# Performance work log

Hardware: AMD Instinct MI355X
Metric: run time of the kernel (lower is better)

Reference implementation:

```python
import jax, jax.numpy as jnp
import numpy as np

BETA = 0.9
THRESHOLD = 1.0
DELTA_THRESH = 0.2  # spikegen.delta threshold in encoder
NUM_STEPS = 64


def heaviside(v):
    return (v > 0).astype(v.dtype)


def lif_layer(cur):
    """snntorch Leaky (reset_mechanism='subtract') over cur: [S, B, H].
    mem_new = beta*mem + cur - (mem_old > thr)*thr ; spk = (mem_new > thr)."""
    def step(mem, c):
        reset = heaviside(mem - THRESHOLD)
        mem_new = BETA * mem + c - reset * THRESHOLD
        spk = heaviside(mem_new - THRESHOLD)
        return mem_new, spk

    mem0 = jnp.zeros(cur.shape[1:], cur.dtype)
    _, spk_rec = jax.lax.scan(step, mem0, cur)
    return spk_rec  # [S, B, H]


def setup_inputs() -> dict:
    key = jax.random.key(0)
    ks = jax.random.split(key, 7)
    F_in, H1, H2, H3 = 512, 1024, 1024, 512
    x = jax.random.normal(ks[0], (256, 128, F_in), dtype=jnp.float32)
    def lin(k, out_d, in_d):
        kw, kb = jax.random.split(k)
        s = 1.0 / np.sqrt(in_d)
        W = jax.random.uniform(kw, (out_d, in_d), jnp.float32, -s, s)
        b = jax.random.uniform(kb, (out_d,), jnp.float32, -s, s)
        return W, b
    W0, b0 = lin(ks[1], H1, F_in)
    W1, b1 = lin(ks[2], H2, H1)
    W2, b2 = lin(ks[3], H3, H2)
    return {"x": x, "W0": W0, "b0": b0, "W1": W1, "b1": b1, "W2": W2, "b2": b2}


def reference(x, W0, b0, W1, b1, W2, b2):
    B, T, F_in = x.shape
    # SpikeEncoder 'delta': spikegen.delta diffs along dim 0 (batch here, faithful to torch call)
    prev = jnp.concatenate([x[:1], x[:-1]], axis=0)
    delta_spk = ((x - prev) >= DELTA_THRESH).astype(x.dtype)  # [B, T, F]
    # repeat over S then mean over T  ==  mean over T then broadcast over S
    spikes = jnp.broadcast_to(delta_spk.mean(axis=1), (NUM_STEPS, B, F_in))  # [S, B, F]
    for W, b in ((W0, b0), (W1, b1), (W2, b2)):
        cur = jnp.einsum('sbf,hf->sbh', spikes, W) + b  # batched fc across all steps
        spikes = lif_layer(cur)
    return spikes  # [S, B, H_last]
```

## Files before the change

### kernel.cpp

```cpp
#include <hip/hip_runtime.h>
#include <hip/hip_bf16.h>

#define S_STEPS 64

typedef __bf16 bf16x8 __attribute__((ext_vector_type(8)));
typedef float  f32x4  __attribute__((ext_vector_type(4)));
typedef int    i32x4  __attribute__((ext_vector_type(4)));

__device__ __forceinline__ void async16(const void* g, void* l) {
    __builtin_amdgcn_global_load_lds((const __attribute__((address_space(1))) void*)g,
                                     (__attribute__((address_space(3))) void*)l,
                                     16, 0, 0);
}

__global__ void snn_encoder_tp(const float4* __restrict__ xv, ushort4* __restrict__ r,
                               int B, int T, int F4) {
    const int f4i = threadIdx.x & 63;
    const int tc  = threadIdx.x >> 6;
    const int b   = blockIdx.y;
    const int f4  = blockIdx.x * 64 + f4i;
    __shared__ int4 red[4][64];

    int c0 = 0, c1 = 0, c2 = 0, c3 = 0;
    if (b > 0) {
        const float4* xb = xv + ((size_t)b * T + tc * 32) * F4 + f4;
        const float4* xp = xb - (size_t)T * F4;
        for (int t = 0; t < 32; ++t) {
            float4 a = xb[(size_t)t * F4];
            float4 p = xp[(size_t)t * F4];
            c0 += (__fsub_rn(a.x, p.x) >= 0.2f) ? 1 : 0;
            c1 += (__fsub_rn(a.y, p.y) >= 0.2f) ? 1 : 0;
            c2 += (__fsub_rn(a.z, p.z) >= 0.2f) ? 1 : 0;
            c3 += (__fsub_rn(a.w, p.w) >= 0.2f) ? 1 : 0;
        }
    }
    red[tc][f4i] = int4{c0, c1, c2, c3};
    __syncthreads();
    if (tc == 0) {
        int4 a = red[0][f4i], bb = red[1][f4i], cc = red[2][f4i], dd = red[3][f4i];
        int s0 = a.x + bb.x + cc.x + dd.x;
        int s1 = a.y + bb.y + cc.y + dd.y;
        int s2 = a.z + bb.z + cc.z + dd.z;
        int s3 = a.w + bb.w + cc.w + dd.w;
        ushort4 o;
        o.x = __hip_bfloat16_raw(__float2bfloat16((float)s0 * (1.0f / 128.0f))).x;
        o.y = __hip_bfloat16_raw(__float2bfloat16((float)s1 * (1.0f / 128.0f))).x;
        o.z = __hip_bfloat16_raw(__float2bfloat16((float)s2 * (1.0f / 128.0f))).x;
        o.w = __hip_bfloat16_raw(__float2bfloat16((float)s3 * (1.0f / 128.0f))).x;
        r[(size_t)b * F4 + f4] = o;
    }
}

__global__ void split_w0_v4(const float4* __restrict__ W, int n4, ushort4* __restrict__ out) {
    int j = blockIdx.x * blockDim.x + threadIdx.x;
    if (j >= n4) return;
    float4 w = W[j];
    float wv[4] = {w.x, w.y, w.z, w.w};
    unsigned short hv[4], mv[4], lv[4];
    #pragma unroll
    for (int q = 0; q < 4; ++q) {
        __hip_bfloat16 hh = __float2bfloat16(wv[q]);
        float r1 = __fsub_rn(wv[q], __bfloat162float(hh));
        __hip_bfloat16 mm = __float2bfloat16(r1);
        float r2 = __fsub_rn(r1, __bfloat162float(mm));
        hv[q] = __hip_bfloat16_raw(hh).x;
        mv[q] = __hip_bfloat16_raw(mm).x;
        lv[q] = __hip_bfloat16_raw(__float2bfloat16(r2)).x;
    }
    out[j]          = ushort4{hv[0], hv[1], hv[2], hv[3]};
    out[j + n4]     = ushort4{mv[0], mv[1], mv[2], mv[3]};
    out[j + 2 * n4] = ushort4{lv[0], lv[1], lv[2], lv[3]};
}

__global__ void quant_w_i8(const float4* __restrict__ Wa, const float4* __restrict__ Wb,
                           int na4, int nb4,
                           char4* __restrict__ outA, char4* __restrict__ outB) {
    int i = blockIdx.x * blockDim.x + threadIdx.x;
    const float4* W; char4* out; int n4; int j = i;
    if (j < na4) { W = Wa; out = outA; n4 = na4; }
    else {
        j -= na4;
        if (j >= nb4) return;
        W = Wb; out = outB; n4 = nb4;
    }
    float4 w = W[j];
    float wv[4] = {w.x, w.y, w.z, w.w};
    signed char d2v[4], d1v[4], d0v[4];
    #pragma unroll
    for (int q = 0; q < 4; ++q) {
        int e  = __float2int_rn(wv[q] * 134217728.0f);
        int d0 = (int)(signed char)(e & 0xff);
        int e1 = (e - d0) >> 8;
        int d1 = (int)(signed char)(e1 & 0xff);
        int d2 = (e1 - d1) >> 8;
        d0v[q] = (signed char)d0;
        d1v[q] = (signed char)d1;
        d2v[q] = (signed char)d2;
    }
    out[j]          = make_char4(d2v[0], d2v[1], d2v[2], d2v[3]);
    out[j + n4]     = make_char4(d1v[0], d1v[1], d1v[2], d1v[3]);
    out[j + 2 * n4] = make_char4(d0v[0], d0v[1], d0v[2], d0v[3]);
}


__global__ __launch_bounds__(256, 2)
void snn_gemm_i8_w_lif(const signed char* __restrict__ A,
                       const signed char* __restrict__ Wq,
                       const float* __restrict__ bias,
                       signed char* __restrict__ Sout,
                       int M, int N, int K) {
    __shared__ __align__(16) char As[3 * 8192];
    __shared__ __align__(16) char Bs[3 * 16384];
    const int t    = threadIdx.x;
    const int wave = t >> 6;
    const int lane = t & 63;

    int m_idx, n_idx;
    {
        int gx = gridDim.x, gy = gridDim.y;
        int flat = blockIdx.y * gx + blockIdx.x;
        if ((gy & 7) == 0) {
            int x = flat & 7, local = flat >> 3, h = gy >> 3;
            m_idx = x * h + (local % h);
            n_idx = local / h;
        } else { m_idx = blockIdx.y; n_idx = blockIdx.x; }
    }
    const int m0 = m_idx * 128;
    const int n0 = n_idx * 256;
    const int wm = (wave >> 1) * 64;
    const int wn = (wave & 1) * 128;

    const int srow = lane >> 2;
    const int schk = ((lane & 3) + (lane >> 2) + (lane >> 4)) & 3;
    const int rho  = lane & 15;
    const int kap  = lane >> 4;
    const int foff = ((rho << 2) + ((kap - rho - (rho >> 2)) & 3)) * 16;

    const int KT = K >> 6;
    const int NT = 3 * KT;
    const size_t PK = (size_t)N * K;

    size_t aOff[2], bOff[4];
    #pragma unroll
    for (int q = 0; q < 2; ++q)
        aOff[q] = (size_t)(m0 + (wave * 2 + q) * 16 + srow) * K + schk * 16;
    #pragma unroll
    for (int q = 0; q < 4; ++q)
        bOff[q] = (size_t)(n0 + (wave * 4 + q) * 16 + srow) * K + schk * 16;

    i32x4 acc[4][8] = {};
    i32x4 afA[4], afB[4], bLo[4], bHi[4];

    auto stageT = [&](int p, int kt, int bsel) {
        const int kk = kt << 6;
        char* as = As + bsel * 8192;
        char* bs = Bs + bsel * 16384;
        #pragma unroll
        for (int q = 0; q < 2; ++q)
            async16(A + aOff[q] + kk, as + (wave * 2 + q) * 1024 + lane * 16);
        const signed char* Bw = Wq + (size_t)p * PK;
        #pragma unroll
        for (int q = 0; q < 4; ++q)
            async16(Bw + bOff[q] + kk, bs + (wave * 4 + q) * 1024 + lane * 16);
    };

    int sp = 0, skt = 2;
    int sbuf = 2, rbuf = 1;

    auto body = [&](int i, i32x4* afc, i32x4* afn) {
        if (i + 2 < NT) {
            stageT(sp, skt, sbuf);
            if (++skt == KT) { skt = 0; ++sp; }
            asm volatile("s_waitcnt vmcnt(6)" ::: "memory");
        } else {
            asm volatile("s_waitcnt vmcnt(0)" ::: "memory");
        }
        __builtin_amdgcn_s_barrier();
        const char* as = As + rbuf * 8192;
        const char* bs = Bs + rbuf * 16384;
        #pragma unroll
        for (int q = 0; q < 4; ++q)
            afn[q] = *(const i32x4*)&as[((wm >> 4) + q) * 1024 + foff];
        #pragma unroll
        for (int q = 0; q < 4; ++q)
            bLo[q] = *(const i32x4*)&bs[((wn >> 4) + q) * 1024 + foff];
        __builtin_amdgcn_sched_barrier(0);
        #pragma unroll
        for (int q = 0; q < 4; ++q)
            #pragma unroll
            for (int j = 0; j < 4; ++j)
                acc[q][4 + j] = __builtin_amdgcn_mfma_i32_16x16x64_i8(afc[q], bHi[j], acc[q][4 + j], 0, 0, 0);
        #pragma unroll
        for (int q = 0; q < 4; ++q)
            bHi[q] = *(const i32x4*)&bs[((wn >> 4) + 4 + q) * 1024 + foff];
        asm volatile("s_waitcnt lgkmcnt(0)" ::: "memory");
        __builtin_amdgcn_sched_barrier(0);
        if (((i + 1) & (KT - 1)) == 0) {
            #pragma unroll
            for (int q = 0; q < 4; ++q)
                #pragma unroll
                for (int j = 0; j < 8; ++j)
                    acc[q][j] = acc[q][j] * 256;
        }
        #pragma unroll
        for (int q = 0; q < 4; ++q)
            #pragma unroll
            for (int j = 0; j < 4; ++j)
                acc[q][j] = __builtin_amdgcn_mfma_i32_16x16x64_i8(afn[q], bLo[j], acc[q][j], 0, 0, 0);
        sbuf = (sbuf == 2) ? 0 : sbuf + 1;
        rbuf = (rbuf == 2) ? 0 : rbuf + 1;
    };

    stageT(0, 0, 0);
    stageT(0, 1, 1);
    asm volatile("s_waitcnt vmcnt(6)" ::: "memory");
    __builtin_amdgcn_s_barrier();
    {
        const char* as = As;
        const char* bs = Bs;
        #pragma unroll
        for (int q = 0; q < 4; ++q)
            afA[q] = *(const i32x4*)&as[((wm >> 4) + q) * 1024 + foff];
        #pragma unroll
        for (int q = 0; q < 4; ++q) {
            bLo[q] = *(const i32x4*)&bs[((wn >> 4) + q) * 1024 + foff];
            bHi[q] = *(const i32x4*)&bs[((wn >> 4) + 4 + q) * 1024 + foff];
        }
    }
    asm volatile("s_waitcnt lgkmcnt(0)" ::: "memory");
    __builtin_amdgcn_sched_barrier(0);
    #pragma unroll
    for (int q = 0; q < 4; ++q)
        #pragma unroll
        for (int j = 0; j < 4; ++j)
            acc[q][j] = __builtin_amdgcn_mfma_i32_16x16x64_i8(afA[q], bLo[j], acc[q][j], 0, 0, 0);

    for (int i = 0; i < NT - 2; i += 2) {
        body(i, afA, afB);
        body(i + 1, afB, afA);
    }
    body(NT - 2, afA, afB);
    #pragma unroll
    for (int q = 0; q < 4; ++q)
        #pragma unroll
        for (int j = 0; j < 4; ++j)
            acc[q][4 + j] = __builtin_amdgcn_mfma_i32_16x16x64_i8(afB[q], bHi[j], acc[q][4 + j], 0, 0, 0);

    const float SCALE = 7.450580596923828e-9f;
    float bb[8];
    #pragma unroll
    for (int j = 0; j < 8; ++j)
        bb[j] = bias[n0 + wn + j * 16 + (lane & 15)];
    #pragma unroll
    for (int i = 0; i < 4; ++i)
        #pragma unroll
        for (int j = 0; j < 8; ++j) {
            i32x4 v = acc[i][j];
            f32x4 c;
            #pragma unroll
            for (int r = 0; r < 4; ++r)
                c[r] = (float)v[r] * SCALE + bb[j];
            acc[i][j] = __builtin_bit_cast(i32x4, c);
        }
    float mj[8] = {0.f, 0.f, 0.f, 0.f, 0.f, 0.f, 0.f, 0.f};
    signed char* So = Sout + (size_t)(m0 + wm) * N;
    #pragma unroll
    for (int seg = 0; seg < 16; ++seg) {
        const int si = seg >> 2, sk = seg & 3;
        const int src = (lane & 15) | (((sk + 3) & 3) << 4);
        #pragma unroll
        for (int j = 0; j < 8; ++j) {
            float tin = __shfl(mj[j], src);
            if (seg > 0 && kap == sk) mj[j] = tin;
        }
        if (kap == sk) {
            #pragma unroll
            for (int j = 0; j < 8; ++j) {
                f32x4 c = __builtin_bit_cast(f32x4, acc[si][j]);
                const int ng = n0 + wn + j * 16 + (lane & 15);
                #pragma unroll
                for (int r = 0; r < 4; ++r) {
                    float rst = (mj[j] > 1.0f) ? 1.0f : 0.0f;
                    mj[j] = __fsub_rn(__fadd_rn(__fmul_rn(0.9f, mj[j]), c[r]), rst);
                    So[(size_t)(seg * 4 + r) * N + ng] = (mj[j] > 1.0f) ? (signed char)1 : (signed char)0;
                }
            }
        }
    }
}

__global__ __launch_bounds__(256, 2)
void snn_gemm_i8_n_lif(const signed char* __restrict__ A,
                       const signed char* __restrict__ Wq,
                       const float* __restrict__ bias,
                       float* __restrict__ Dout,
                       int M, int N, int K, int Bsz) {
    __shared__ __align__(16) char As[3 * 8192];
    __shared__ __align__(16) char Bs[3 * 8192];
    const int t    = threadIdx.x;
    const int wave = t >> 6;
    const int lane = t & 63;

    int m_idx, n_idx;
    {
        int gx = gridDim.x, gy = gridDim.y;
        int flat = blockIdx.y * gx + blockIdx.x;
        if ((gy & 7) == 0) {
            int x = flat & 7, local = flat >> 3, h = gy >> 3;
            m_idx = x * h + (local % h);
            n_idx = local / h;
        } else { m_idx = blockIdx.y; n_idx = blockIdx.x; }
    }
    const int m0 = m_idx * 128;
    const int n0 = n_idx * 128;
    const int wm = (wave & 1) * 64;
    const int wn = (wave >> 1) * 64;

    const int srow = lane >> 2;
    const int schk = ((lane & 3) + (lane >> 2) + (lane >> 4)) & 3;
    const int rho  = lane & 15;
    const int kap  = lane >> 4;
    const int foff = ((rho << 2) + ((kap - rho - (rho >> 2)) & 3)) * 16;

    const int KT = K >> 6;
    const int NT = 3 * KT;
    const size_t PK = (size_t)N * K;

    size_t aOff[2], bOff[2];
    #pragma unroll
    for (int q = 0; q < 2; ++q) {
        aOff[q] = (size_t)(m0 + (wave * 2 + q) * 16 + srow) * K + schk * 16;
        bOff[q] = (size_t)(n0 + (wave * 2 + q) * 16 + srow) * K + schk * 16;
    }

    i32x4 acc[4][4] = {};
    i32x4 afA[4], afB[4], bLo[2], bHi[2];

    auto stageT = [&](int p, int kt, int bsel) {
        const int kk = kt << 6;
        char* as = As + bsel * 8192;
        char* bs = Bs + bsel * 8192;
        const signed char* Bw = Wq + (size_t)p * PK;
        #pragma unroll
        for (int q = 0; q < 2; ++q) {
            async16(A  + aOff[q] + kk, as + (wave * 2 + q) * 1024 + lane * 16);
            async16(Bw + bOff[q] + kk, bs + (wave * 2 + q) * 1024 + lane * 16);
        }
    };

    int sp = 0, skt = 2;
    int sbuf = 2, rbuf = 1;

    auto body = [&](int i, i32x4* afc, i32x4* afn) {
        if (i + 2 < NT) {
            stageT(sp, skt, sbuf);
            if (++skt == KT) { skt = 0; ++sp; }
            asm volatile("s_waitcnt vmcnt(4)" ::: "memory");
        } else {
            asm volatile("s_waitcnt vmcnt(0)" ::: "memory");
        }
        __builtin_amdgcn_s_barrier();
        const char* as = As + rbuf * 8192;
        const char* bs = Bs + rbuf * 8192;
        #pragma unroll
        for (int q = 0; q < 4; ++q)
            afn[q] = *(const i32x4*)&as[((wm >> 4) + q) * 1024 + foff];
        #pragma unroll
        for (int q = 0; q < 2; ++q)
            bLo[q] = *(const i32x4*)&bs[((wn >> 4) + q) * 1024 + foff];
        __builtin_amdgcn_sched_barrier(0);
        #pragma unroll
        for (int q = 0; q < 4; ++q)
            #pragma unroll
            for (int j = 0; j < 2; ++j)
                acc[q][2 + j] = __builtin_amdgcn_mfma_i32_16x16x64_i8(afc[q], bHi[j], acc[q][2 + j], 0, 0, 0);
        #pragma unroll
        for (int q = 0; q < 2; ++q)
            bHi[q] = *(const i32x4*)&bs[((wn >> 4) + 2 + q) * 1024 + foff];
        asm volatile("s_waitcnt lgkmcnt(0)" ::: "memory");
        __builtin_amdgcn_sched_barrier(0);
        if (((i + 1) & (KT - 1)) == 0) {
            #pragma unroll
            for (int q = 0; q < 4; ++q)
                #pragma unroll
                for (int j = 0; j < 4; ++j)
                    acc[q][j] = acc[q][j] * 256;
        }
        #pragma unroll
        for (int q = 0; q < 4; ++q)
            #pragma unroll
            for (int j = 0; j < 2; ++j)
                acc[q][j] = __builtin_amdgcn_mfma_i32_16x16x64_i8(afn[q], bLo[j], acc[q][j], 0, 0, 0);
        sbuf = (sbuf == 2) ? 0 : sbuf + 1;
        rbuf = (rbuf == 2) ? 0 : rbuf + 1;
    };

    stageT(0, 0, 0);
    stageT(0, 1, 1);
    asm volatile("s_waitcnt vmcnt(4)" ::: "memory");
    __builtin_amdgcn_s_barrier();
    {
        const char* as = As;
        const char* bs = Bs;
        #pragma unroll
        for (int q = 0; q < 4; ++q)
            afA[q] = *(const i32x4*)&as[((wm >> 4) + q) * 1024 + foff];
        #pragma unroll
        for (int q = 0; q < 2; ++q) {
            bLo[q] = *(const i32x4*)&bs[((wn >> 4) + q) * 1024 + foff];
            bHi[q] = *(const i32x4*)&bs[((wn >> 4) + 2 + q) * 1024 + foff];
        }
    }
    asm volatile("s_waitcnt lgkmcnt(0)" ::: "memory");
    __builtin_amdgcn_sched_barrier(0);
    #pragma unroll
    for (int q = 0; q < 4; ++q)
        #pragma unroll
        for (int j = 0; j < 2; ++j)
            acc[q][j] = __builtin_amdgcn_mfma_i32_16x16x64_i8(afA[q], bLo[j], acc[q][j], 0, 0, 0);

    for (int i = 0; i < NT - 2; i += 2) {
        body(i, afA, afB);
        body(i + 1, afB, afA);
    }
    body(NT - 2, afA, afB);
    #pragma unroll
    for (int q = 0; q < 4; ++q)
        #pragma unroll
        for (int j = 0; j < 2; ++j)
            acc[q][2 + j] = __builtin_amdgcn_mfma_i32_16x16x64_i8(afB[q], bHi[j], acc[q][2 + j], 0, 0, 0);

    const float SCALE = 7.450580596923828e-9f;
    float bb[4];
    #pragma unroll
    for (int j = 0; j < 4; ++j)
        bb[j] = bias[n0 + wn + j * 16 + (lane & 15)];
    #pragma unroll
    for (int i = 0; i < 4; ++i)
        #pragma unroll
        for (int j = 0; j < 4; ++j) {
            i32x4 v = acc[i][j];
            f32x4 c;
            #pragma unroll
            for (int r = 0; r < 4; ++r)
                c[r] = (float)v[r] * SCALE + bb[j];
            acc[i][j] = __builtin_bit_cast(i32x4, c);
        }
    float mj[4] = {0.f, 0.f, 0.f, 0.f};
    const int b_idx = (m0 + wm) >> 6;
    #pragma unroll
    for (int seg = 0; seg < 16; ++seg) {
        const int si = seg >> 2, sk = seg & 3;
        const int src = (lane & 15) | (((sk + 3) & 3) << 4);
        #pragma unroll
        for (int j = 0; j < 4; ++j) {
            float tin = __shfl(mj[j], src);
            if (seg > 0 && kap == sk) mj[j] = tin;
        }
        if (kap == sk) {
            #pragma unroll
            for (int j = 0; j < 4; ++j) {
                f32x4 c = __builtin_bit_cast(f32x4, acc[si][j]);
                const int ng = n0 + wn + j * 16 + (lane & 15);
                #pragma unroll
                for (int r = 0; r < 4; ++r) {
                    float rst = (mj[j] > 1.0f) ? 1.0f : 0.0f;
                    mj[j] = __fsub_rn(__fadd_rn(__fmul_rn(0.9f, mj[j]), c[r]), rst);
                    Dout[((size_t)(seg * 4 + r) * Bsz + b_idx) * N + ng] = (mj[j] > 1.0f) ? 1.0f : 0.0f;
                }
            }
        }
    }
}

__global__ __launch_bounds__(256)
void snn_gemm_mfma_n(const __hip_bfloat16* __restrict__ A,
                     const __hip_bfloat16* __restrict__ Whi,
                     const __hip_bfloat16* __restrict__ Wmid,
                     const __hip_bfloat16* __restrict__ Wlo,
                     const float* __restrict__ bias,
                     float* __restrict__ C,
                     int M, int N, int K) {
    __shared__ __align__(16) unsigned short As[128 * 32];
    __shared__ __align__(16) unsigned short Bs[128 * 32];
    const int t    = threadIdx.x;
    const int wave = t >> 6;
    const int lane = t & 63;

    int m_idx = blockIdx.y, n_idx = blockIdx.x;
    const int m0 = m_idx * 128;
    const int n0 = n_idx * 128;
    const int wm = (wave & 1) * 64;
    const int wn = (wave >> 1) * 64;

    const int srow = lane >> 2;
    const int schk = ((lane & 3) + (lane >> 2) + (lane >> 4)) & 3;
    const int rho  = lane & 15;
    const int kap  = lane >> 4;
    const int foff = ((rho << 2) + ((kap - rho - (rho >> 2)) & 3)) * 8;

    f32x4 acc[4][4] = {};

    const __hip_bfloat16* parts[3] = {Whi, Wmid, Wlo};
    for (int part = 0; part < 3; ++part) {
        const __hip_bfloat16* Bw = parts[part];
        for (int k0 = 0; k0 < K; k0 += 32) {
            __syncthreads();
            #pragma unroll
            for (int q = 0; q < 2; ++q) {
                int grp = wave * 2 + q;
                async16(A  + (size_t)(m0 + grp * 16 + srow) * K + k0 + schk * 8,
                        &As[grp * 512 + lane * 8]);
                async16(Bw + (size_t)(n0 + grp * 16 + srow) * K + k0 + schk * 8,
                        &Bs[grp * 512 + lane * 8]);
            }
            __syncthreads();

            bf16x8 af[4], bfr[4];
            #pragma unroll
            for (int i = 0; i < 4; ++i) {
                af[i]  = *(const bf16x8*)&As[((wm >> 4) + i) * 512 + foff];
                bfr[i] = *(const bf16x8*)&Bs[((wn >> 4) + i) * 512 + foff];
            }
            #pragma unroll
            for (int i = 0; i < 4; ++i)
                #pragma unroll
                for (int j = 0; j < 4; ++j)
                    acc[i][j] = __builtin_amdgcn_mfma_f32_16x16x32_bf16(af[i], bfr[j], acc[i][j], 0, 0, 0);
        }
    }

    #pragma unroll
    for (int i = 0; i < 4; ++i) {
        int mg = m0 + wm + i * 16 + (lane >> 4) * 4;
        #pragma unroll
        for (int j = 0; j < 4; ++j) {
            int ng = n0 + wn + j * 16 + (lane & 15);
            float bb = bias[ng];
            #pragma unroll
            for (int r = 0; r < 4; ++r)
                C[(size_t)(mg + r) * N + ng] = acc[i][j][r] + bb;
        }
    }
}

__global__ void snn_lif0_i8_bmaj(const float4* __restrict__ cur, uchar4* __restrict__ spk,
                                 int BH4, int H4) {
    int idx = blockIdx.x * blockDim.x + threadIdx.x;
    if (idx >= BH4) return;
    const int b  = idx / H4;
    const int h4 = idx - b * H4;
    uchar4* out = spk + (size_t)b * S_STEPS * H4 + h4;
    float m0 = 0.0f, m1 = 0.0f, m2 = 0.0f, m3 = 0.0f;
    float4 c = cur[idx];
    for (int s = 0; s < S_STEPS; ++s) {
        float r0 = (m0 > 1.0f) ? 1.0f : 0.0f;
        float r1 = (m1 > 1.0f) ? 1.0f : 0.0f;
        float r2 = (m2 > 1.0f) ? 1.0f : 0.0f;
        float r3 = (m3 > 1.0f) ? 1.0f : 0.0f;
        m0 = __fsub_rn(__fadd_rn(__fmul_rn(0.9f, m0), c.x), r0);
        m1 = __fsub_rn(__fadd_rn(__fmul_rn(0.9f, m1), c.y), r1);
        m2 = __fsub_rn(__fadd_rn(__fmul_rn(0.9f, m2), c.z), r2);
        m3 = __fsub_rn(__fadd_rn(__fmul_rn(0.9f, m3), c.w), r3);
        uchar4 o;
        o.x = (m0 > 1.0f) ? 1 : 0;
        o.y = (m1 > 1.0f) ? 1 : 0;
        o.z = (m2 > 1.0f) ? 1 : 0;
        o.w = (m3 > 1.0f) ? 1 : 0;
        out[(size_t)s * H4] = o;
    }
}

extern "C" void kernel_launch(void* const* d_in, const int* in_sizes, int n_in,
                              void* d_out, int out_size, void* d_ws, size_t ws_size,
                              hipStream_t stream) {
    const float* x  = (const float*)d_in[0];
    const float* W0 = (const float*)d_in[1];
    const float* b0 = (const float*)d_in[2];
    const float* W1 = (const float*)d_in[3];
    const float* b1 = (const float*)d_in[4];
    const float* W2 = (const float*)d_in[5];
    const float* b2 = (const float*)d_in[6];

    const int B = 256, T = 128, F = 512, H1 = 1024, H2 = 1024, H3 = 512;
    const int SB = S_STEPS * B;

    char* w = (char*)d_ws;
    signed char*    spk0 = (signed char*)w;                 w += (size_t)SB * H1;
    signed char*    spk1 = (signed char*)w;                 w += (size_t)SB * H2;
    __hip_bfloat16* r_bf = (__hip_bfloat16*)w;              w += (size_t)B * F * 2;
    float*          cur0 = (float*)w;                       w += (size_t)B * H1 * 4;
    __hip_bfloat16* W0s  = (__hip_bfloat16*)w;              w += (size_t)3 * H1 * F * 2;
    signed char*    W1q  = (signed char*)w;                 w += (size_t)3 * H2 * H1;
    signed char*    W2q  = (signed char*)w;                 w += (size_t)3 * H3 * H2;

    const int nW0 = H1 * F, nW1 = H2 * H1, nW2 = H3 * H2;

    split_w0_v4<<<dim3((nW0 / 4 + 255) / 256), dim3(256), 0, stream>>>(
        (const float4*)W0, nW0 / 4, (ushort4*)W0s);

    {
        int n4 = (nW1 + nW2) / 4;
        quant_w_i8<<<dim3((n4 + 255) / 256), dim3(256), 0, stream>>>(
            (const float4*)W1, (const float4*)W2, nW1 / 4, nW2 / 4,
            (char4*)W1q, (char4*)W2q);
    }

    snn_encoder_tp<<<dim3(F / 4 / 64, B), dim3(256), 0, stream>>>(
        (const float4*)x, (ushort4*)r_bf, B, T, F / 4);

    snn_gemm_mfma_n<<<dim3(H1 / 128, B / 128), dim3(256), 0, stream>>>(
        r_bf, W0s, W0s + nW0, W0s + 2 * nW0, b0, cur0, B, H1, F);

    snn_lif0_i8_bmaj<<<dim3(B * H1 / 4 / 256), dim3(256), 0, stream>>>(
        (const float4*)cur0, (uchar4*)spk0, B * H1 / 4, H1 / 4);

    snn_gemm_i8_w_lif<<<dim3(H2 / 256, SB / 128), dim3(256), 0, stream>>>(
        spk0, W1q, b1, spk1, SB, H2, H1);

    snn_gemm_i8_n_lif<<<dim3(H3 / 128, SB / 128), dim3(256), 0, stream>>>(
        spk1, W2q, b2, (float*)d_out, SB, H3, H2, B);
}
```

Baseline: 258.2 us.

## Merge prep kernels into one launch and fully unroll int8 GEMM K-loops

Folds the encoder, W0 bf16 split and W1/W2 int8 quantization kernels into a single block-partitioned prep kernel, removing two launches and letting the independent work run concurrently. The two int8 GEMM+LIF kernels now take compile-time N/K constants and fully unroll the pipelined K loop with constant buffer indices instead of runtime rotating counters. This removes launch gaps and index arithmetic, but the much larger unrolled code may raise instruction-cache pressure and compile time. It also hardcodes the problem shape.

```diff
diff --git a/kernel.cpp b/kernel.cpp
--- a/kernel.cpp
+++ b/kernel.cpp
@@ -13,93 +13,93 @@
                                      16, 0, 0);
 }
 
-__global__ void snn_encoder_tp(const float4* __restrict__ xv, ushort4* __restrict__ r,
-                               int B, int T, int F4) {
-    const int f4i = threadIdx.x & 63;
-    const int tc  = threadIdx.x >> 6;
-    const int b   = blockIdx.y;
-    const int f4  = blockIdx.x * 64 + f4i;
+__global__ void snn_prep(const float4* __restrict__ xv, ushort4* __restrict__ r,
+                         const float4* __restrict__ W0, ushort4* __restrict__ w0out,
+                         const float4* __restrict__ W1, const float4* __restrict__ W2,
+                         char4* __restrict__ w1out, char4* __restrict__ w2out) {
+    constexpr int T = 128, F4 = 128;
+    constexpr int NB_ENC = 512;
+    constexpr int N0_4 = 1024 * 512 / 4;
+    constexpr int NB_W0 = N0_4 / 256;
+    constexpr int N1_4 = 1024 * 1024 / 4;
+    constexpr int N2_4 = 512 * 1024 / 4;
     __shared__ int4 red[4][64];
 
-    int c0 = 0, c1 = 0, c2 = 0, c3 = 0;
-    if (b > 0) {
-        const float4* xb = xv + ((size_t)b * T + tc * 32) * F4 + f4;
-        const float4* xp = xb - (size_t)T * F4;
-        for (int t = 0; t < 32; ++t) {
-            float4 a = xb[(size_t)t * F4];
-            float4 p = xp[(size_t)t * F4];
-            c0 += (__fsub_rn(a.x, p.x) >= 0.2f) ? 1 : 0;
-            c1 += (__fsub_rn(a.y, p.y) >= 0.2f) ? 1 : 0;
-            c2 += (__fsub_rn(a.z, p.z) >= 0.2f) ? 1 : 0;
-            c3 += (__fsub_rn(a.w, p.w) >= 0.2f) ? 1 : 0;
-        }
-    }
-    red[tc][f4i] = int4{c0, c1, c2, c3};
-    __syncthreads();
-    if (tc == 0) {
-        int4 a = red[0][f4i], bb = red[1][f4i], cc = red[2][f4i], dd = red[3][f4i];
-        int s0 = a.x + bb.x + cc.x + dd.x;
-        int s1 = a.y + bb.y + cc.y + dd.y;
-        int s2 = a.z + bb.z + cc.z + dd.z;
-        int s3 = a.w + bb.w + cc.w + dd.w;
-        ushort4 o;
-        o.x = __hip_bfloat16_raw(__float2bfloat16((float)s0 * (1.0f / 128.0f))).x;
-        o.y = __hip_bfloat16_raw(__float2bfloat16((float)s1 * (1.0f / 128.0f))).x;
-        o.z = __hip_bfloat16_raw(__float2bfloat16((float)s2 * (1.0f / 128.0f))).x;
-        o.w = __hip_bfloat16_raw(__float2bfloat16((float)s3 * (1.0f / 128.0f))).x;
-        r[(size_t)b * F4 + f4] = o;
-    }
-}
-
-__global__ void split_w0_v4(const float4* __restrict__ W, int n4, ushort4* __restrict__ out) {
-    int j = blockIdx.x * blockDim.x + threadIdx.x;
-    if (j >= n4) return;
-    float4 w = W[j];
-    float wv[4] = {w.x, w.y, w.z, w.w};
-    unsigned short hv[4], mv[4], lv[4];
-    #pragma unroll
-    for (int q = 0; q < 4; ++q) {
-        __hip_bfloat16 hh = __float2bfloat16(wv[q]);
-        float r1 = __fsub_rn(wv[q], __bfloat162float(hh));
-        __hip_bfloat16 mm = __float2bfloat16(r1);
-        float r2 = __fsub_rn(r1, __bfloat162float(mm));
-        hv[q] = __hip_bfloat16_raw(hh).x;
-        mv[q] = __hip_bfloat16_raw(mm).x;
-        lv[q] = __hip_bfloat16_raw(__float2bfloat16(r2)).x;
-    }
-    out[j]          = ushort4{hv[0], hv[1], hv[2], hv[3]};
-    out[j + n4]     = ushort4{mv[0], mv[1], mv[2], mv[3]};
-    out[j + 2 * n4] = ushort4{lv[0], lv[1], lv[2], lv[3]};
-}
-
-__global__ void quant_w_i8(const float4* __restrict__ Wa, const float4* __restrict__ Wb,
-                           int na4, int nb4,
-                           char4* __restrict__ outA, char4* __restrict__ outB) {
-    int i = blockIdx.x * blockDim.x + threadIdx.x;
-    const float4* W; char4* out; int n4; int j = i;
-    if (j < na4) { W = Wa; out = outA; n4 = na4; }
-    else {
-        j -= na4;
-        if (j >= nb4) return;
-        W = Wb; out = outB; n4 = nb4;
-    }
-    float4 w = W[j];
-    float wv[4] = {w.x, w.y, w.z, w.w};
-    signed char d2v[4], d1v[4], d0v[4];
-    #pragma unroll
-    for (int q = 0; q < 4; ++q) {
-        int e  = __float2int_rn(wv[q] * 134217728.0f);
-        int d0 = (int)(signed char)(e & 0xff);
-        int e1 = (e - d0) >> 8;
-        int d1 = (int)(signed char)(e1 & 0xff);
-        int d2 = (e1 - d1) >> 8;
-        d0v[q] = (signed char)d0;
-        d1v[q] = (signed char)d1;
-        d2v[q] = (signed char)d2;
-    }
-    out[j]          = make_char4(d2v[0], d2v[1], d2v[2], d2v[3]);
-    out[j + n4]     = make_char4(d1v[0], d1v[1], d1v[2], d1v[3]);
-    out[j + 2 * n4] = make_char4(d0v[0], d0v[1], d0v[2], d0v[3]);
+    const int bid = blockIdx.x;
+    if (bid < NB_ENC) {
+        const int f4i = threadIdx.x & 63;
+        const int tc  = threadIdx.x >> 6;
+        const int b   = bid >> 1;
+        const int f4  = (bid & 1) * 64 + f4i;
+        int c0 = 0, c1 = 0, c2 = 0, c3 = 0;
+        if (b > 0) {
+            const float4* xb = xv + ((size_t)b * T + tc * 32) * F4 + f4;
+            const float4* xp = xb - (size_t)T * F4;
+            for (int t = 0; t < 32; ++t) {
+                float4 a = xb[(size_t)t * F4];
+                float4 p = xp[(size_t)t * F4];
+                c0 += (__fsub_rn(a.x, p.x) >= 0.2f) ? 1 : 0;
+                c1 += (__fsub_rn(a.y, p.y) >= 0.2f) ? 1 : 0;
+                c2 += (__fsub_rn(a.z, p.z) >= 0.2f) ? 1 : 0;
+                c3 += (__fsub_rn(a.w, p.w) >= 0.2f) ? 1 : 0;
+            }
+        }
+        red[tc][f4i] = int4{c0, c1, c2, c3};
+        __syncthreads();
+        if (tc == 0) {
+            int4 a = red[0][f4i], bb = red[1][f4i], cc = red[2][f4i], dd = red[3][f4i];
+            int s0 = a.x + bb.x + cc.x + dd.x;
+            int s1 = a.y + bb.y + cc.y + dd.y;
+            int s2 = a.z + bb.z + cc.z + dd.z;
+            int s3 = a.w + bb.w + cc.w + dd.w;
+            ushort4 o;
+            o.x = __hip_bfloat16_raw(__float2bfloat16((float)s0 * (1.0f / 128.0f))).x;
+            o.y = __hip_bfloat16_raw(__float2bfloat16((float)s1 * (1.0f / 128.0f))).x;
+            o.z = __hip_bfloat16_raw(__float2bfloat16((float)s2 * (1.0f / 128.0f))).x;
+            o.w = __hip_bfloat16_raw(__float2bfloat16((float)s3 * (1.0f / 128.0f))).x;
+            r[(size_t)b * F4 + f4] = o;
+        }
+    } else if (bid < NB_ENC + NB_W0) {
+        int j = (bid - NB_ENC) * 256 + threadIdx.x;
+        float4 w = W0[j];
+        float wv[4] = {w.x, w.y, w.z, w.w};
+        unsigned short hv[4], mv[4], lv[4];
+        #pragma unroll
+        for (int q = 0; q < 4; ++q) {
+            __hip_bfloat16 hh = __float2bfloat16(wv[q]);
+            float r1 = __fsub_rn(wv[q], __bfloat162float(hh));
+            __hip_bfloat16 mm = __float2bfloat16(r1);
+            float r2 = __fsub_rn(r1, __bfloat162float(mm));
+            hv[q] = __hip_bfloat16_raw(hh).x;
+            mv[q] = __hip_bfloat16_raw(mm).x;
+            lv[q] = __hip_bfloat16_raw(__float2bfloat16(r2)).x;
+        }
+        w0out[j]             = ushort4{hv[0], hv[1], hv[2], hv[3]};
+        w0out[j + N0_4]      = ushort4{mv[0], mv[1], mv[2], mv[3]};
+        w0out[j + 2 * N0_4]  = ushort4{lv[0], lv[1], lv[2], lv[3]};
+    } else {
+        int i = (bid - NB_ENC - NB_W0) * 256 + threadIdx.x;
+        const float4* W; char4* out; int n4; int j = i;
+        if (j < N1_4) { W = W1; out = w1out; n4 = N1_4; }
+        else { j -= N1_4; W = W2; out = w2out; n4 = N2_4; }
+        float4 w = W[j];
+        float wv[4] = {w.x, w.y, w.z, w.w};
+        signed char d2v[4], d1v[4], d0v[4];
+        #pragma unroll
+        for (int q = 0; q < 4; ++q) {
+            int e  = __float2int_rn(wv[q] * 134217728.0f);
+            int d0 = (int)(signed char)(e & 0xff);
+            int e1 = (e - d0) >> 8;
+            int d1 = (int)(signed char)(e1 & 0xff);
+            int d2 = (e1 - d1) >> 8;
+            d0v[q] = (signed char)d0;
+            d1v[q] = (signed char)d1;
+            d2v[q] = (signed char)d2;
+        }
+        out[j]          = make_char4(d2v[0], d2v[1], d2v[2], d2v[3]);
+        out[j + n4]     = make_char4(d1v[0], d1v[1], d1v[2], d1v[3]);
+        out[j + 2 * n4] = make_char4(d0v[0], d0v[1], d0v[2], d0v[3]);
+    }
 }
 
 
@@ -107,8 +107,9 @@
 void snn_gemm_i8_w_lif(const signed char* __restrict__ A,
                        const signed char* __restrict__ Wq,
                        const float* __restrict__ bias,
-                       signed char* __restrict__ Sout,
-                       int M, int N, int K) {
+                       signed char* __restrict__ Sout) {
+    constexpr int N = 1024, K = 1024, KT = K >> 6, NT = 3 * KT;
+    constexpr size_t PK = (size_t)N * K;
     __shared__ __align__(16) char As[3 * 8192];
     __shared__ __align__(16) char Bs[3 * 16384];
     const int t    = threadIdx.x;
@@ -136,10 +137,6 @@
     const int kap  = lane >> 4;
     const int foff = ((rho << 2) + ((kap - rho - (rho >> 2)) & 3)) * 16;
 
-    const int KT = K >> 6;
-    const int NT = 3 * KT;
-    const size_t PK = (size_t)N * K;
-
     size_t aOff[2], bOff[4];
     #pragma unroll
     for (int q = 0; q < 2; ++q)
@@ -149,7 +146,7 @@
         bOff[q] = (size_t)(n0 + (wave * 4 + q) * 16 + srow) * K + schk * 16;
 
     i32x4 acc[4][8] = {};
-    i32x4 afA[4], afB[4], bLo[4], bHi[4];
+    i32x4 af[2][4], bLo[4], bHi[4];
 
     auto stageT = [&](int p, int kt, int bsel) {
         const int kk = kt << 6;
@@ -164,23 +161,41 @@
             async16(Bw + bOff[q] + kk, bs + (wave * 4 + q) * 1024 + lane * 16);
     };
 
-    int sp = 0, skt = 2;
-    int sbuf = 2, rbuf = 1;
-
-    auto body = [&](int i, i32x4* afc, i32x4* afn) {
-        if (i + 2 < NT) {
-            stageT(sp, skt, sbuf);
-            if (++skt == KT) { skt = 0; ++sp; }
+    stageT(0, 0, 0);
+    stageT(0, 1, 1);
+    asm volatile("s_waitcnt vmcnt(6)" ::: "memory");
+    __builtin_amdgcn_s_barrier();
+    #pragma unroll
+    for (int q = 0; q < 4; ++q)
+        af[0][q] = *(const i32x4*)&As[((wm >> 4) + q) * 1024 + foff];
+    #pragma unroll
+    for (int q = 0; q < 4; ++q) {
+        bLo[q] = *(const i32x4*)&Bs[((wn >> 4) + q) * 1024 + foff];
+        bHi[q] = *(const i32x4*)&Bs[((wn >> 4) + 4 + q) * 1024 + foff];
+    }
+    asm volatile("s_waitcnt lgkmcnt(0)" ::: "memory");
+    __builtin_amdgcn_sched_barrier(0);
+    #pragma unroll
+    for (int q = 0; q < 4; ++q)
+        #pragma unroll
+        for (int j = 0; j < 4; ++j)
+            acc[q][j] = __builtin_amdgcn_mfma_i32_16x16x64_i8(af[0][q], bLo[j], acc[q][j], 0, 0, 0);
+
+    #pragma unroll
+    for (int i = 0; i < NT - 1; ++i) {
+        const int nt = i + 2;
+        if (nt < NT) {
+            stageT(nt / KT, nt % KT, nt % 3);
             asm volatile("s_waitcnt vmcnt(6)" ::: "memory");
         } else {
             asm volatile("s_waitcnt vmcnt(0)" ::: "memory");
         }
         __builtin_amdgcn_s_barrier();
-        const char* as = As + rbuf * 8192;
-        const char* bs = Bs + rbuf * 16384;
-        #pragma unroll
-        for (int q = 0; q < 4; ++q)
-            afn[q] = *(const i32x4*)&as[((wm >> 4) + q) * 1024 + foff];
+        const char* as = As + ((i + 1) % 3) * 8192;
+        const char* bs = Bs + ((i + 1) % 3) * 16384;
+        #pragma unroll
+        for (int q = 0; q < 4; ++q)
+            af[(i + 1) & 1][q] = *(const i32x4*)&as[((wm >> 4) + q) * 1024 + foff];
         #pragma unroll
         for (int q = 0; q < 4; ++q)
             bLo[q] = *(const i32x4*)&bs[((wn >> 4) + q) * 1024 + foff];
@@ -189,13 +204,13 @@
         for (int q = 0; q < 4; ++q)
             #pragma unroll
             for (int j = 0; j < 4; ++j)
-                acc[q][4 + j] = __builtin_amdgcn_mfma_i32_16x16x64_i8(afc[q], bHi[j], acc[q][4 + j], 0, 0, 0);
+                acc[q][4 + j] = __builtin_amdgcn_mfma_i32_16x16x64_i8(af[i & 1][q], bHi[j], acc[q][4 + j], 0, 0, 0);
         #pragma unroll
         for (int q = 0; q < 4; ++q)
             bHi[q] = *(const i32x4*)&bs[((wn >> 4) + 4 + q) * 1024 + foff];
         asm volatile("s_waitcnt lgkmcnt(0)" ::: "memory");
         __builtin_amdgcn_sched_barrier(0);
-        if (((i + 1) & (KT - 1)) == 0) {
+        if (((i + 1) % KT) == 0) {
             #pragma unroll
             for (int q = 0; q < 4; ++q)
                 #pragma unroll
@@ -206,45 +221,13 @@
         for (int q = 0; q < 4; ++q)
             #pragma unroll
             for (int j = 0; j < 4; ++j)
-                acc[q][j] = __builtin_amdgcn_mfma_i32_16x16x64_i8(afn[q], bLo[j], acc[q][j], 0, 0, 0);
-        sbuf = (sbuf == 2) ? 0 : sbuf + 1;
-        rbuf = (rbuf == 2) ? 0 : rbuf + 1;
-    };
-
-    stageT(0, 0, 0);
-    stageT(0, 1, 1);
-    asm volatile("s_waitcnt vmcnt(6)" ::: "memory");
-    __builtin_amdgcn_s_barrier();
-    {
-        const char* as = As;
-        const char* bs = Bs;
-        #pragma unroll
-        for (int q = 0; q < 4; ++q)
-            afA[q] = *(const i32x4*)&as[((wm >> 4) + q) * 1024 + foff];
-        #pragma unroll
-        for (int q = 0; q < 4; ++q) {
-            bLo[q] = *(const i32x4*)&bs[((wn >> 4) + q) * 1024 + foff];
-            bHi[q] = *(const i32x4*)&bs[((wn >> 4) + 4 + q) * 1024 + foff];
-        }
-    }
-    asm volatile("s_waitcnt lgkmcnt(0)" ::: "memory");
-    __builtin_amdgcn_sched_barrier(0);
+                acc[q][j] = __builtin_amdgcn_mfma_i32_16x16x64_i8(af[(i + 1) & 1][q], bLo[j], acc[q][j], 0, 0, 0);
+    }
     #pragma unroll
     for (int q = 0; q < 4; ++q)
         #pragma unroll
         for (int j = 0; j < 4; ++j)
-            acc[q][j] = __builtin_amdgcn_mfma_i32_16x16x64_i8(afA[q], bLo[j], acc[q][j], 0, 0, 0);
-
-    for (int i = 0; i < NT - 2; i += 2) {
-        body(i, afA, afB);
-        body(i + 1, afB, afA);
-    }
-    body(NT - 2, afA, afB);
-    #pragma unroll
-    for (int q = 0; q < 4; ++q)
-        #pragma unroll
-        for (int j = 0; j < 4; ++j)
-            acc[q][4 + j] = __builtin_amdgcn_mfma_i32_16x16x64_i8(afB[q], bHi[j], acc[q][4 + j], 0, 0, 0);
+            acc[q][4 + j] = __builtin_amdgcn_mfma_i32_16x16x64_i8(af[(NT - 1) & 1][q], bHi[j], acc[q][4 + j], 0, 0, 0);
 
     const float SCALE = 7.450580596923828e-9f;
     float bb[8];
@@ -293,8 +276,10 @@
 void snn_gemm_i8_n_lif(const signed char* __restrict__ A,
                        const signed char* __restrict__ Wq,
                        const float* __restrict__ bias,
-                       float* __restrict__ Dout,
-                       int M, int N, int K, int Bsz) {
+                       float* __restrict__ Dout) {
+    constexpr int N = 512, K = 1024, KT = K >> 6, NT = 3 * KT;
+    constexpr int BSZ = 256;
+    constexpr size_t PK = (size_t)N * K;
     __shared__ __align__(16) char As[3 * 8192];
     __shared__ __align__(16) char Bs[3 * 8192];
     const int t    = threadIdx.x;
@@ -322,10 +307,6 @@
     const int kap  = lane >> 4;
     const int foff = ((rho << 2) + ((kap - rho - (rho >> 2)) & 3)) * 16;
 
-    const int KT = K >> 6;
-    const int NT = 3 * KT;
-    const size_t PK = (size_t)N * K;
-
     size_t aOff[2], bOff[2];
     #pragma unroll
     for (int q = 0; q < 2; ++q) {
@@ -334,7 +315,7 @@
     }
 
     i32x4 acc[4][4] = {};
-    i32x4 afA[4], afB[4], bLo[2], bHi[2];
+    i32x4 af[2][4], bLo[2], bHi[2];
 
     auto stageT = [&](int p, int kt, int bsel) {
         const int kk = kt << 6;
@@ -348,23 +329,41 @@
         }
     };
 
-    int sp = 0, skt = 2;
-    int sbuf = 2, rbuf = 1;
-
-    auto body = [&](int i, i32x4* afc, i32x4* afn) {
-        if (i + 2 < NT) {
-            stageT(sp, skt, sbuf);
-            if (++skt == KT) { skt = 0; ++sp; }
+    stageT(0, 0, 0);
+    stageT(0, 1, 1);
+    asm volatile("s_waitcnt vmcnt(4)" ::: "memory");
+    __builtin_amdgcn_s_barrier();
+    #pragma unroll
+    for (int q = 0; q < 4; ++q)
+        af[0][q] = *(const i32x4*)&As[((wm >> 4) + q) * 1024 + foff];
+    #pragma unroll
+    for (int q = 0; q < 2; ++q) {
+        bLo[q] = *(const i32x4*)&Bs[((wn >> 4) + q) * 1024 + foff];
+        bHi[q] = *(const i32x4*)&Bs[((wn >> 4) + 2 + q) * 1024 + foff];
+    }
+    asm volatile("s_waitcnt lgkmcnt(0)" ::: "memory");
+    __builtin_amdgcn_sched_barrier(0);
+    #pragma unroll
+    for (int q = 0; q < 4; ++q)
+        #pragma unroll
+        for (int j = 0; j < 2; ++j)
+            acc[q][j] = __builtin_amdgcn_mfma_i32_16x16x64_i8(af[0][q], bLo[j], acc[q][j], 0, 0, 0);
+
+    #pragma unroll
+    for (int i = 0; i < NT - 1; ++i) {
+        const int nt = i + 2;
+        if (nt < NT) {
+            stageT(nt / KT, nt % KT, nt % 3);
             asm volatile("s_waitcnt vmcnt(4)" ::: "memory");
         } else {
             asm volatile("s_waitcnt vmcnt(0)" ::: "memory");
         }
         __builtin_amdgcn_s_barrier();
-        const char* as = As + rbuf * 8192;
-        const char* bs = Bs + rbuf * 8192;
-        #pragma unroll
-        for (int q = 0; q < 4; ++q)
-            afn[q] = *(const i32x4*)&as[((wm >> 4) + q) * 1024 + foff];
+        const char* as = As + ((i + 1) % 3) * 8192;
+        const char* bs = Bs + ((i + 1) % 3) * 8192;
+        #pragma unroll
+        for (int q = 0; q < 4; ++q)
+            af[(i + 1) & 1][q] = *(const i32x4*)&as[((wm >> 4) + q) * 1024 + foff];
         #pragma unroll
         for (int q = 0; q < 2; ++q)
             bLo[q] = *(const i32x4*)&bs[((wn >> 4) + q) * 1024 + foff];
@@ -373,13 +372,13 @@
         for (int q = 0; q < 4; ++q)
             #pragma unroll
             for (int j = 0; j < 2; ++j)
-                acc[q][2 + j] = __builtin_amdgcn_mfma_i32_16x16x64_i8(afc[q], bHi[j], acc[q][2 + j], 0, 0, 0);
+                acc[q][2 + j] = __builtin_amdgcn_mfma_i32_16x16x64_i8(af[i & 1][q], bHi[j], acc[q][2 + j], 0, 0, 0);
         #pragma unroll
         for (int q = 0; q < 2; ++q)
             bHi[q] = *(const i32x4*)&bs[((wn >> 4) + 2 + q) * 1024 + foff];
         asm volatile("s_waitcnt lgkmcnt(0)" ::: "memory");
         __builtin_amdgcn_sched_barrier(0);
-        if (((i + 1) & (KT - 1)) == 0) {
+        if (((i + 1) % KT) == 0) {
             #pragma unroll
             for (int q = 0; q < 4; ++q)
                 #pragma unroll
@@ -390,45 +389,13 @@
         for (int q = 0; q < 4; ++q)
             #pragma unroll
             for (int j = 0; j < 2; ++j)
-                acc[q][j] = __builtin_amdgcn_mfma_i32_16x16x64_i8(afn[q], bLo[j], acc[q][j], 0, 0, 0);
-        sbuf = (sbuf == 2) ? 0 : sbuf + 1;
-        rbuf = (rbuf == 2) ? 0 : rbuf + 1;
-    };
-
-    stageT(0, 0, 0);
-    stageT(0, 1, 1);
-    asm volatile("s_waitcnt vmcnt(4)" ::: "memory");
-    __builtin_amdgcn_s_barrier();
-    {
-        const char* as = As;
-        const char* bs = Bs;
-        #pragma unroll
-        for (int q = 0; q < 4; ++q)
-            afA[q] = *(const i32x4*)&as[((wm >> 4) + q) * 1024 + foff];
-        #pragma unroll
-        for (int q = 0; q < 2; ++q) {
-            bLo[q] = *(const i32x4*)&bs[((wn >> 4) + q) * 1024 + foff];
-            bHi[q] = *(const i32x4*)&bs[((wn >> 4) + 2 + q) * 1024 + foff];
-        }
-    }
-    asm volatile("s_waitcnt lgkmcnt(0)" ::: "memory");
-    __builtin_amdgcn_sched_barrier(0);
+                acc[q][j] = __builtin_amdgcn_mfma_i32_16x16x64_i8(af[(i + 1) & 1][q], bLo[j], acc[q][j], 0, 0, 0);
+    }
     #pragma unroll
     for (int q = 0; q < 4; ++q)
         #pragma unroll
         for (int j = 0; j < 2; ++j)
-            acc[q][j] = __builtin_amdgcn_mfma_i32_16x16x64_i8(afA[q], bLo[j], acc[q][j], 0, 0, 0);
-
-    for (int i = 0; i < NT - 2; i += 2) {
-        body(i, afA, afB);
-        body(i + 1, afB, afA);
-    }
-    body(NT - 2, afA, afB);
-    #pragma unroll
-    for (int q = 0; q < 4; ++q)
-        #pragma unroll
-        for (int j = 0; j < 2; ++j)
-            acc[q][2 + j] = __builtin_amdgcn_mfma_i32_16x16x64_i8(afB[q], bHi[j], acc[q][2 + j], 0, 0, 0);
+            acc[q][2 + j] = __builtin_amdgcn_mfma_i32_16x16x64_i8(af[(NT - 1) & 1][q], bHi[j], acc[q][2 + j], 0, 0, 0);
 
     const float SCALE = 7.450580596923828e-9f;
     float bb[4];
@@ -466,7 +433,7 @@
                 for (int r = 0; r < 4; ++r) {
                     float rst = (mj[j] > 1.0f) ? 1.0f : 0.0f;
                     mj[j] = __fsub_rn(__fadd_rn(__fmul_rn(0.9f, mj[j]), c[r]), rst);
-                    Dout[((size_t)(seg * 4 + r) * Bsz + b_idx) * N + ng] = (mj[j] > 1.0f) ? 1.0f : 0.0f;
+                    Dout[((size_t)(seg * 4 + r) * BSZ + b_idx) * N + ng] = (mj[j] > 1.0f) ? 1.0f : 0.0f;
                 }
             }
         }
@@ -594,20 +561,13 @@
     signed char*    W1q  = (signed char*)w;                 w += (size_t)3 * H2 * H1;
     signed char*    W2q  = (signed char*)w;                 w += (size_t)3 * H3 * H2;
 
-    const int nW0 = H1 * F, nW1 = H2 * H1, nW2 = H3 * H2;
-
-    split_w0_v4<<<dim3((nW0 / 4 + 255) / 256), dim3(256), 0, stream>>>(
-        (const float4*)W0, nW0 / 4, (ushort4*)W0s);
-
-    {
-        int n4 = (nW1 + nW2) / 4;
-        quant_w_i8<<<dim3((n4 + 255) / 256), dim3(256), 0, stream>>>(
-            (const float4*)W1, (const float4*)W2, nW1 / 4, nW2 / 4,
-            (char4*)W1q, (char4*)W2q);
-    }
-
-    snn_encoder_tp<<<dim3(F / 4 / 64, B), dim3(256), 0, stream>>>(
-        (const float4*)x, (ushort4*)r_bf, B, T, F / 4);
+    const int nW0 = H1 * F;
+
+    snn_prep<<<dim3(2560), dim3(256), 0, stream>>>(
+        (const float4*)x, (ushort4*)r_bf,
+        (const float4*)W0, (ushort4*)W0s,
+        (const float4*)W1, (const float4*)W2,
+        (char4*)W1q, (char4*)W2q);
 
     snn_gemm_mfma_n<<<dim3(H1 / 128, B / 128), dim3(256), 0, stream>>>(
         r_bf, W0s, W0s + nW0, W0s + 2 * nW0, b0, cur0, B, H1, F);
@@ -616,8 +576,8 @@
         (const float4*)cur0, (uchar4*)spk0, B * H1 / 4, H1 / 4);
 
     snn_gemm_i8_w_lif<<<dim3(H2 / 256, SB / 128), dim3(256), 0, stream>>>(
-        spk0, W1q, b1, spk1, SB, H2, H1);
+        spk0, W1q, b1, spk1);
 
     snn_gemm_i8_n_lif<<<dim3(H3 / 128, SB / 128), dim3(256), 0, stream>>>(
-        spk1, W2q, b2, (float*)d_out, SB, H3, H2, B);
-}
+        spk1, W2q, b2, (float*)d_out);
+}
```

Result: slower. 265.0 us (+2.6%).
